# Kernel optimization log

Measured on AMD Instinct MI355X. Metric: run time of the kernel, lower is better.

The kernel has to match this reference:

```python
import jax, jax.numpy as jnp
import numpy as np

N_NODES = 100000
N_EDGES = 1600000
IN_FEAT = 50
HIDDEN = 64
N_CLASSES = 41


def setup_inputs() -> dict:
    key = jax.random.key(0)
    ks = jax.random.split(key, 8)
    x = jax.random.normal(ks[0], (N_NODES, IN_FEAT), dtype=jnp.float32)
    W1_l = jax.random.normal(ks[1], (IN_FEAT, HIDDEN), dtype=jnp.float32) * (1.0 / np.sqrt(IN_FEAT))
    W1_r = jax.random.normal(ks[2], (IN_FEAT, HIDDEN), dtype=jnp.float32) * (1.0 / np.sqrt(IN_FEAT))
    b1 = jnp.zeros((HIDDEN,), dtype=jnp.float32)
    W2_l = jax.random.normal(ks[3], (HIDDEN, N_CLASSES), dtype=jnp.float32) * (1.0 / np.sqrt(HIDDEN))
    W2_r = jax.random.normal(ks[4], (HIDDEN, N_CLASSES), dtype=jnp.float32) * (1.0 / np.sqrt(HIDDEN))
    b2 = jnp.zeros((N_CLASSES,), dtype=jnp.float32)
    src = jax.random.randint(ks[5], (N_EDGES,), 0, N_NODES, dtype=jnp.int64 if jax.config.jax_enable_x64 else jnp.int32)
    dst = jax.random.randint(ks[6], (N_EDGES,), 0, N_NODES, dtype=jnp.int64 if jax.config.jax_enable_x64 else jnp.int32)
    return {"x": x, "W1_l": W1_l, "W1_r": W1_r, "b1": b1,
            "W2_l": W2_l, "W2_r": W2_r, "b2": b2, "src": src, "dst": dst}


def _sage_conv(h, src, dst, W_l, W_r, b):
    # sum-aggregate neighbor features (message from src -> dst), then dense transform
    agg = jax.ops.segment_sum(h[src], dst, num_segments=N_NODES)  # [N, F]
    return agg @ W_l + h @ W_r + b


def reference(x, W1_l, W1_r, b1, W2_l, W2_r, b2, src, dst):
    h = _sage_conv(x, src, dst, W1_l, W1_r, b1)
    h = jax.nn.relu(h)
    # dropout is identity in eval mode
    o = _sage_conv(h, src, dst, W2_l, W2_r, b2)
    return jax.nn.log_softmax(o, axis=1)
```

## Files before the change

### kernel.cpp

```cpp
#include <hip/hip_runtime.h>
#include <hip/hip_bf16.h>
#include <math.h>

#define N_NODES   100000
#define N_EDGES   1600000
#define IN_FEAT   50
#define HIDDEN    64
#define N_CLASSES 41
#define NC48      48
#define N_TILES   (N_NODES / 16)

#define NPB   200
#define NBUK  (N_NODES / NPB)
#define BEPT  16
#define BA_BLOCKS ((N_EDGES + 256 * BEPT - 1) / (256 * BEPT))
#define SCAP  4096

typedef __attribute__((ext_vector_type(8))) _Float16 half8;
typedef __attribute__((ext_vector_type(4))) float   float4v;

union f16pk { _Float16 h[2]; unsigned u; };
union quadpk { uint4 v; _Float16 h[8]; };

__device__ __forceinline__ int clampidx(int i) {
  return ((unsigned)i < (unsigned)N_NODES) ? i : 0;
}

__device__ __forceinline__ void acc8(float* acc, const quadpk& u, float one) {
#pragma unroll
  for (int t = 0; t < 8; ++t) acc[t] = fmaf((float)u.h[t], one, acc[t]);
}

__global__ __launch_bounds__(256) void packx_kernel(
    const float* __restrict__ x, _Float16* __restrict__ xh) {
  int i = blockIdx.x * 256 + threadIdx.x;
  if (i >= N_NODES * 64) return;
  int node = i >> 6, c = i & 63;
  xh[i] = (c < IN_FEAT) ? (_Float16)x[node * IN_FEAT + c] : (_Float16)0.f;
}

__global__ __launch_bounds__(256) void packwts_kernel(
    const float* __restrict__ W1l, const float* __restrict__ W1r,
    const float* __restrict__ W2l, const float* __restrict__ W2r,
    unsigned* __restrict__ wt1l, unsigned* __restrict__ wt1r,
    unsigned* __restrict__ wt2l, unsigned* __restrict__ wt2r,
    int* __restrict__ bcnt) {
  if (blockIdx.x == 0) {
    for (int j = threadIdx.x; j < 512; j += 256) bcnt[j] = 0;
  }
  int i = blockIdx.x * 256 + threadIdx.x;
  f16pk pk;
  if (i < 2048 * 2) {
    int which = i >> 11, j = i & 2047;
    int n = j >> 5, kp = j & 31;
    const float* W = which ? W1r : W1l;
    int k0 = 2 * kp, k1 = 2 * kp + 1;
    pk.h[0] = (_Float16)((k0 < IN_FEAT) ? W[k0 * HIDDEN + n] : 0.f);
    pk.h[1] = (_Float16)((k1 < IN_FEAT) ? W[k1 * HIDDEN + n] : 0.f);
    (which ? wt1r : wt1l)[j] = pk.u;
  } else if (i < 4096 + 2 * 1536) {
    int j = i - 4096;
    int which = (j >= 1536), jj = which ? j - 1536 : j;
    int n = jj >> 5, kp = jj & 31;
    const float* W = which ? W2r : W2l;
    pk.h[0] = (_Float16)((n < N_CLASSES) ? W[(2 * kp) * N_CLASSES + n] : 0.f);
    pk.h[1] = (_Float16)((n < N_CLASSES) ? W[(2 * kp + 1) * N_CLASSES + n] : 0.f);
    (which ? wt2r : wt2l)[jj] = pk.u;
  }
}

__global__ __launch_bounds__(256) void bhist_kernel(
    const int* __restrict__ dst, int* __restrict__ bcnt) {
  __shared__ int lh[NBUK];
  int tid = threadIdx.x;
  for (int i = tid; i < NBUK; i += 256) lh[i] = 0;
  __syncthreads();
  int base = blockIdx.x * (256 * BEPT);
#pragma unroll
  for (int k = 0; k < BEPT; ++k) {
    int e = base + k * 256 + tid;
    if (e < N_EDGES) {
      int d = clampidx(dst[e]);
      atomicAdd(&lh[(unsigned)d / (unsigned)NPB], 1);
    }
  }
  __syncthreads();
  for (int i = tid; i < NBUK; i += 256)
    if (lh[i]) atomicAdd(&bcnt[i], lh[i]);
}

__global__ __launch_bounds__(256) void bscan_kernel(
    const int* __restrict__ bcnt, int* __restrict__ wbase,
    int* __restrict__ wcur, int* __restrict__ start) {
  __shared__ int lds[256];
  int tid = threadIdx.x;
  int i0 = 2 * tid, i1 = 2 * tid + 1;
  int a0 = (i0 < NBUK) ? bcnt[i0] : 0;
  int a1 = (i1 < NBUK) ? bcnt[i1] : 0;
  int s = a0 + a1;
  lds[tid] = s;
  __syncthreads();
  for (int off = 1; off < 256; off <<= 1) {
    int t = (tid >= off) ? lds[tid - off] : 0;
    __syncthreads();
    lds[tid] += t;
    __syncthreads();
  }
  int excl = lds[tid] - s;
  if (i0 < NBUK) { wbase[i0] = excl;      wcur[i0] = excl; }
  if (i1 < NBUK) { wbase[i1] = excl + a0; wcur[i1] = excl + a0; }
  if (tid == 0) { wbase[NBUK] = N_EDGES; start[N_NODES] = N_EDGES; }
}

__global__ __launch_bounds__(256) void bucketA_kernel(
    const int* __restrict__ src, const int* __restrict__ dst,
    int* __restrict__ wcur, int2* __restrict__ pairs) {
  __shared__ int lcnt[NBUK];
  __shared__ int lbase[NBUK];
  int tid = threadIdx.x;
  for (int i = tid; i < NBUK; i += 256) lcnt[i] = 0;
  __syncthreads();
  int base = blockIdx.x * (256 * BEPT);
  int s[BEPT], d[BEPT], rk[BEPT];
#pragma unroll
  for (int k = 0; k < BEPT; ++k) {
    int e = base + k * 256 + tid;
    rk[k] = -1;
    if (e < N_EDGES) {
      s[k] = src[e];
      d[k] = clampidx(dst[e]);
      int w = (unsigned)d[k] / (unsigned)NPB;
      rk[k] = atomicAdd(&lcnt[w], 1);
    }
  }
  __syncthreads();
  for (int i = tid; i < NBUK; i += 256)
    lbase[i] = atomicAdd(&wcur[i], lcnt[i]);
  __syncthreads();
#pragma unroll
  for (int k = 0; k < BEPT; ++k) {
    if (rk[k] >= 0) {
      int w = (unsigned)d[k] / (unsigned)NPB;
      int pos = lbase[w] + rk[k];
      if ((unsigned)pos < (unsigned)N_EDGES) {
        int2 p; p.x = s[k]; p.y = d[k];
        pairs[pos] = p;
      }
    }
  }
}

__global__ __launch_bounds__(256) void sort2_kernel(
    const int2* __restrict__ pairs, const int* __restrict__ wbase,
    int* __restrict__ start, int* __restrict__ ssrc) {
  __shared__ int obuf[SCAP];
  __shared__ int lhist[NPB];
  __shared__ int lcur[NPB];
  __shared__ int lscan[256];
  int b = blockIdx.x;
  int nbase = b * NPB;
  int lo = wbase[b];
  int hi = wbase[b + 1];
  int ne = hi - lo;
  int tid = threadIdx.x;
  for (int i = tid; i < NPB; i += 256) lhist[i] = 0;
  __syncthreads();
  for (int i = lo + tid; i < hi; i += 256) {
    int2 p = pairs[i];
    unsigned li = (unsigned)(p.y - nbase);
    if (li < (unsigned)NPB) atomicAdd(&lhist[li], 1);
  }
  __syncthreads();
  int hv = (tid < NPB) ? lhist[tid] : 0;
  lscan[tid] = hv;
  __syncthreads();
  for (int off = 1; off < 256; off <<= 1) {
    int t = (tid >= off) ? lscan[tid - off] : 0;
    __syncthreads();
    lscan[tid] += t;
    __syncthreads();
  }
  if (tid < NPB) {
    int excl = lscan[tid] - hv;
    lcur[tid] = excl;
    unsigned sidx = (unsigned)(nbase + tid);
    if (sidx < (unsigned)N_NODES) start[sidx] = lo + excl;
  }
  __syncthreads();
  if (ne >= 0 && ne <= SCAP) {
    for (int i = lo + tid; i < hi; i += 256) {
      int2 p = pairs[i];
      unsigned li = (unsigned)(p.y - nbase);
      if (li < (unsigned)NPB) {
        int pos = atomicAdd(&lcur[li], 1);
        if ((unsigned)pos < (unsigned)SCAP) obuf[pos] = p.x;
      }
    }
    __syncthreads();
    for (int i = tid; i < ne; i += 256) {
      unsigned gi = (unsigned)(lo + i);
      if (gi < (unsigned)N_EDGES) ssrc[gi] = obuf[i];
    }
  } else {
    for (int i = lo + tid; i < hi; i += 256) {
      int2 p = pairs[i];
      unsigned li = (unsigned)(p.y - nbase);
      if (li < (unsigned)NPB) {
        int pos = atomicAdd(&lcur[li], 1);
        unsigned gi = (unsigned)(lo + pos);
        if (gi < (unsigned)N_EDGES) ssrc[gi] = p.x;
      }
    }
  }
}

__global__ __launch_bounds__(256) void g1mlp_kernel(
    const uint4* __restrict__ xq,
    const int* __restrict__ start, const int* __restrict__ ssrc,
    const _Float16* __restrict__ xh,
    const unsigned* __restrict__ wt1l, const unsigned* __restrict__ wt1r,
    const unsigned* __restrict__ wt2l, const unsigned* __restrict__ wt2r,
    const float* __restrict__ b1, const float* __restrict__ b2,
    _Float16* __restrict__ hlh, float* __restrict__ opart, float one) {
  __shared__ float aggF[16][64];
  __shared__ float sH[16][68];
  int tile = blockIdx.x;
  int wv = threadIdx.x >> 6;
  int lane = threadIdx.x & 63;
  int r = lane >> 3, q = lane & 7;

  for (int k = 0; k < 4; ++k) {
    int node = tile * 16 + wv * 4 + k;

    float accA[8] = {0.f, 0.f, 0.f, 0.f, 0.f, 0.f, 0.f, 0.f};
    float accB[8] = {0.f, 0.f, 0.f, 0.f, 0.f, 0.f, 0.f, 0.f};

    int s0 = start[node], s1 = start[node + 1];
    for (int base = s0; base < s1; base += 64) {
      int cnt = s1 - base;
      if (cnt > 64) cnt = 64;
      int idxv = (lane < cnt) ? ssrc[base + lane] : 0;
      int j = 0;
      for (; j + 16 <= cnt; j += 16) {
        int iA = clampidx(__shfl(idxv, j + r));
        int iB = clampidx(__shfl(idxv, j + 8 + r));
        quadpk uA, uB;
        uA.v = xq[iA * 8 + q];
        uB.v = xq[iB * 8 + q];
        acc8(accA, uA, one);
        acc8(accB, uB, one);
      }
      for (; j + 8 <= cnt; j += 8) {
        int iA = clampidx(__shfl(idxv, j + r));
        quadpk uA;
        uA.v = xq[iA * 8 + q];
        acc8(accA, uA, one);
      }
      if (j < cnt) {
        int nrem = cnt - j;
        int iA = clampidx(__shfl(idxv, j + r));
        if (r < nrem) {
          quadpk uA;
          uA.v = xq[iA * 8 + q];
          acc8(accA, uA, one);
        }
      }
    }
#pragma unroll
    for (int t = 0; t < 8; ++t) accA[t] += accB[t];
#pragma unroll
    for (int off = 8; off <= 32; off <<= 1) {
#pragma unroll
      for (int t = 0; t < 8; ++t) accA[t] += __shfl_xor(accA[t], off);
    }
    if (r == 0) {
      int nl = wv * 4 + k;
#pragma unroll
      for (int t = 0; t < 8; ++t) aggF[nl][q * 8 + t] = accA[t];
    }
  }
  __syncthreads();

  if (wv != 0) return;
  int m = lane & 15, quad = lane >> 4;

  half8 Aa[2], Ax[2];
#pragma unroll
  for (int s = 0; s < 2; ++s) {
    const float* pa = &aggF[m][s * 32 + quad * 8];
    half8 A;
#pragma unroll
    for (int jj = 0; jj < 8; ++jj) A[jj] = (_Float16)pa[jj];
    Aa[s] = A;
    Ax[s] = *(const half8*)(xh + (tile * 16 + m) * 64 + s * 32 + quad * 8);
  }

#pragma unroll
  for (int t = 0; t < 4; ++t) {
    int n = t * 16 + m;
    half8 Bl0 = *(const half8*)(wt1l + n * 32 + quad * 4);
    half8 Bl1 = *(const half8*)(wt1l + n * 32 + 16 + quad * 4);
    half8 Br0 = *(const half8*)(wt1r + n * 32 + quad * 4);
    half8 Br1 = *(const half8*)(wt1r + n * 32 + 16 + quad * 4);
    float4v acc = {0.f, 0.f, 0.f, 0.f};
    acc = __builtin_amdgcn_mfma_f32_16x16x32_f16(Aa[0], Bl0, acc, 0, 0, 0);
    acc = __builtin_amdgcn_mfma_f32_16x16x32_f16(Aa[1], Bl1, acc, 0, 0, 0);
    acc = __builtin_amdgcn_mfma_f32_16x16x32_f16(Ax[0], Br0, acc, 0, 0, 0);
    acc = __builtin_amdgcn_mfma_f32_16x16x32_f16(Ax[1], Br1, acc, 0, 0, 0);
    float bv = b1[n];
#pragma unroll
    for (int rr = 0; rr < 4; ++rr) {
      sH[quad * 4 + rr][n] = fmaxf(acc[rr] + bv, 0.f);
    }
  }

  half8 Ah[2];
#pragma unroll
  for (int s = 0; s < 2; ++s) {
    const float* pr = &sH[m][s * 32 + quad * 8];
    half8 A;
#pragma unroll
    for (int jj = 0; jj < 8; ++jj) A[jj] = (_Float16)pr[jj];
    Ah[s] = A;
  }

#pragma unroll
  for (int t = 0; t < 3; ++t) {
    int n = t * 16 + m;
    half8 Cl0 = *(const half8*)(wt2l + n * 32 + quad * 4);
    half8 Cl1 = *(const half8*)(wt2l + n * 32 + 16 + quad * 4);
    half8 Cr0 = *(const half8*)(wt2r + n * 32 + quad * 4);
    half8 Cr1 = *(const half8*)(wt2r + n * 32 + 16 + quad * 4);
    float4v acc2 = {0.f, 0.f, 0.f, 0.f};
    float4v acc3 = {0.f, 0.f, 0.f, 0.f};
    acc2 = __builtin_amdgcn_mfma_f32_16x16x32_f16(Ah[0], Cl0, acc2, 0, 0, 0);
    acc2 = __builtin_amdgcn_mfma_f32_16x16x32_f16(Ah[1], Cl1, acc2, 0, 0, 0);
    acc3 = __builtin_amdgcn_mfma_f32_16x16x32_f16(Ah[0], Cr0, acc3, 0, 0, 0);
    acc3 = __builtin_amdgcn_mfma_f32_16x16x32_f16(Ah[1], Cr1, acc3, 0, 0, 0);
    float bv = (n < N_CLASSES) ? b2[n] : 0.f;
#pragma unroll
    for (int rr = 0; rr < 4; ++rr) {
      int row = tile * 16 + quad * 4 + rr;
      hlh[row * NC48 + n] = (_Float16)acc2[rr];
      opart[row * NC48 + n] = acc3[rr] + bv;
    }
  }
}

__global__ __launch_bounds__(256) void gather2_kernel(
    const uint4* __restrict__ hq,
    const float4* __restrict__ opart4,
    const int* __restrict__ start, const int* __restrict__ ssrc,
    float* __restrict__ out, float one) {
  int node = (blockIdx.x * 256 + threadIdx.x) >> 6;
  if (node >= N_NODES) return;
  int lane = threadIdx.x & 63;
  int r = lane >> 3, q = lane & 7;
  bool qOK = (q < 6);

  float op[8] = {0.f, 0.f, 0.f, 0.f, 0.f, 0.f, 0.f, 0.f};
  if (r == 0 && qOK) {
    float4 a = opart4[node * 12 + q * 2];
    float4 b = opart4[node * 12 + q * 2 + 1];
    op[0] = a.x; op[1] = a.y; op[2] = a.z; op[3] = a.w;
    op[4] = b.x; op[5] = b.y; op[6] = b.z; op[7] = b.w;
  }

  float accA[8] = {0.f, 0.f, 0.f, 0.f, 0.f, 0.f, 0.f, 0.f};
  float accB[8] = {0.f, 0.f, 0.f, 0.f, 0.f, 0.f, 0.f, 0.f};

  int s0 = start[node], s1 = start[node + 1];
  for (int base = s0; base < s1; base += 64) {
    int cnt = s1 - base;
    if (cnt > 64) cnt = 64;
    int idxv = (lane < cnt) ? ssrc[base + lane] : 0;
    int j = 0;
    for (; j + 16 <= cnt; j += 16) {
      int iA = clampidx(__shfl(idxv, j + r));
      int iB = clampidx(__shfl(idxv, j + 8 + r));
      if (qOK) {
        quadpk uA, uB;
        uA.v = hq[iA * 6 + q];
        uB.v = hq[iB * 6 + q];
        acc8(accA, uA, one);
        acc8(accB, uB, one);
      }
    }
    for (; j + 8 <= cnt; j += 8) {
      int iA = clampidx(__shfl(idxv, j + r));
      if (qOK) {
        quadpk uA;
        uA.v = hq[iA * 6 + q];
        acc8(accA, uA, one);
      }
    }
    if (j < cnt) {
      int nrem = cnt - j;
      int iA = clampidx(__shfl(idxv, j + r));
      if (r < nrem && qOK) {
        quadpk uA;
        uA.v = hq[iA * 6 + q];
        acc8(accA, uA, one);
      }
    }
  }
#pragma unroll
  for (int t = 0; t < 8; ++t) accA[t] += accB[t];
#pragma unroll
  for (int off = 8; off <= 32; off <<= 1) {
#pragma unroll
    for (int t = 0; t < 8; ++t) accA[t] += __shfl_xor(accA[t], off);
  }

  bool own = (r == 0) && qOK;
  float o[8];
  float lmax = -INFINITY;
#pragma unroll
  for (int t = 0; t < 8; ++t) {
    int f = q * 8 + t;
    o[t] = op[t] + accA[t];
    if (own && f < N_CLASSES) lmax = fmaxf(lmax, o[t]);
  }
  float vm = own ? lmax : -INFINITY;
#pragma unroll
  for (int off = 4; off >= 1; off >>= 1) vm = fmaxf(vm, __shfl_xor(vm, off));
  float lsum = 0.f;
#pragma unroll
  for (int t = 0; t < 8; ++t) {
    int f = q * 8 + t;
    if (own && f < N_CLASSES) lsum += expf(o[t] - vm);
  }
#pragma unroll
  for (int off = 4; off >= 1; off >>= 1) lsum += __shfl_xor(lsum, off);
  float lse = logf(lsum);
  if (own) {
#pragma unroll
    for (int t = 0; t < 8; ++t) {
      int f = q * 8 + t;
      if (f < N_CLASSES) out[node * N_CLASSES + f] = o[t] - vm - lse;
    }
  }
}

extern "C" void kernel_launch(void* const* d_in, const int* in_sizes, int n_in,
                              void* d_out, int out_size, void* d_ws, size_t ws_size,
                              hipStream_t stream) {
  const float* x   = (const float*)d_in[0];
  const float* W1l = (const float*)d_in[1];
  const float* W1r = (const float*)d_in[2];
  const float* b1  = (const float*)d_in[3];
  const float* W2l = (const float*)d_in[4];
  const float* W2r = (const float*)d_in[5];
  const float* b2  = (const float*)d_in[6];
  const int*   src = (const int*)d_in[7];
  const int*   dst = (const int*)d_in[8];
  float* out = (float*)d_out;

  int* counts  = (int*)d_ws;
  int* start   = counts + N_NODES;
  int* cursor  = start + (N_NODES + 1);
  int* partial = cursor + N_NODES;
  int* ssrc    = partial + 64;
  unsigned* wt1l = (unsigned*)(ssrc + N_EDGES);
  unsigned* wt1r = wt1l + 2048;
  unsigned* wt2l = wt1r + 2048;
  unsigned* wt2r = wt2l + 1536;
  uintptr_t pal = ((uintptr_t)(wt2r + 1536) + 255) & ~(uintptr_t)255;
  float* opart   = (float*)pal;
  _Float16* xh   = (_Float16*)(opart + (size_t)N_NODES * NC48);
  _Float16* hlh  = xh + (size_t)N_NODES * 64;

  int* bcnt  = counts;
  int* wbase = counts + 512;

  int2* pairs = (int2*)opart;
  int*  wcur  = (int*)(pairs + N_EDGES);

  packx_kernel<<<(N_NODES * 64 + 255) / 256, 256, 0, stream>>>(x, xh);
  packwts_kernel<<<(7168 + 255) / 256, 256, 0, stream>>>(
      W1l, W1r, W2l, W2r, wt1l, wt1r, wt2l, wt2r, bcnt);
  bhist_kernel<<<BA_BLOCKS, 256, 0, stream>>>(dst, bcnt);
  bscan_kernel<<<1, 256, 0, stream>>>(bcnt, wbase, wcur, start);
  bucketA_kernel<<<BA_BLOCKS, 256, 0, stream>>>(src, dst, wcur, pairs);
  sort2_kernel<<<NBUK, 256, 0, stream>>>(pairs, wbase, start, ssrc);

  g1mlp_kernel<<<N_TILES, 256, 0, stream>>>(
      (const uint4*)xh, start, ssrc, xh, wt1l, wt1r, wt2l, wt2r,
      b1, b2, hlh, opart, 1.0f);

  int gblocks = (N_NODES * 64 + 255) / 256;
  gather2_kernel<<<gblocks, 256, 0, stream>>>(
      (const uint4*)hlh, (const float4*)opart, start, ssrc, out, 1.0f);
}
```

Baseline: 248.6 us.

## Pack edge pairs into single ints and simplify gather index loading

Bucketing now stores each edge as one 32-bit word, with the source node in the upper bits and the destination's offset within its bucket in the low 8 bits. This halves the intermediate pair traffic written by bucketA and read twice by sort2. Both gather kernels drop the 64-wide index load plus shuffle broadcast and instead have each lane group load its edge index directly, 16 edges per step. This removes the shuffles and the remainder loops, at the cost of redundant per-lane index loads.

```diff
diff --git a/kernel.cpp b/kernel.cpp
--- a/kernel.cpp
+++ b/kernel.cpp
@@ -114,23 +114,24 @@
 
 __global__ __launch_bounds__(256) void bucketA_kernel(
     const int* __restrict__ src, const int* __restrict__ dst,
-    int* __restrict__ wcur, int2* __restrict__ pairs) {
+    int* __restrict__ wcur, int* __restrict__ pairs) {
   __shared__ int lcnt[NBUK];
   __shared__ int lbase[NBUK];
   int tid = threadIdx.x;
   for (int i = tid; i < NBUK; i += 256) lcnt[i] = 0;
   __syncthreads();
   int base = blockIdx.x * (256 * BEPT);
-  int s[BEPT], d[BEPT], rk[BEPT];
+  int pk[BEPT], w[BEPT], rk[BEPT];
 #pragma unroll
   for (int k = 0; k < BEPT; ++k) {
     int e = base + k * 256 + tid;
     rk[k] = -1;
     if (e < N_EDGES) {
-      s[k] = src[e];
-      d[k] = clampidx(dst[e]);
-      int w = (unsigned)d[k] / (unsigned)NPB;
-      rk[k] = atomicAdd(&lcnt[w], 1);
+      int s = clampidx(src[e]);
+      int d = clampidx(dst[e]);
+      w[k] = (unsigned)d / (unsigned)NPB;
+      pk[k] = (s << 8) | (d - w[k] * NPB);
+      rk[k] = atomicAdd(&lcnt[w[k]], 1);
     }
   }
   __syncthreads();
@@ -140,18 +141,14 @@
 #pragma unroll
   for (int k = 0; k < BEPT; ++k) {
     if (rk[k] >= 0) {
-      int w = (unsigned)d[k] / (unsigned)NPB;
-      int pos = lbase[w] + rk[k];
-      if ((unsigned)pos < (unsigned)N_EDGES) {
-        int2 p; p.x = s[k]; p.y = d[k];
-        pairs[pos] = p;
-      }
+      int pos = lbase[w[k]] + rk[k];
+      if ((unsigned)pos < (unsigned)N_EDGES) pairs[pos] = pk[k];
     }
   }
 }
 
 __global__ __launch_bounds__(256) void sort2_kernel(
-    const int2* __restrict__ pairs, const int* __restrict__ wbase,
+    const int* __restrict__ pairs, const int* __restrict__ wbase,
     int* __restrict__ start, int* __restrict__ ssrc) {
   __shared__ int obuf[SCAP];
   __shared__ int lhist[NPB];
@@ -166,8 +163,7 @@
   for (int i = tid; i < NPB; i += 256) lhist[i] = 0;
   __syncthreads();
   for (int i = lo + tid; i < hi; i += 256) {
-    int2 p = pairs[i];
-    unsigned li = (unsigned)(p.y - nbase);
+    unsigned li = (unsigned)pairs[i] & 255u;
     if (li < (unsigned)NPB) atomicAdd(&lhist[li], 1);
   }
   __syncthreads();
@@ -189,11 +185,11 @@
   __syncthreads();
   if (ne >= 0 && ne <= SCAP) {
     for (int i = lo + tid; i < hi; i += 256) {
-      int2 p = pairs[i];
-      unsigned li = (unsigned)(p.y - nbase);
+      int p = pairs[i];
+      unsigned li = (unsigned)p & 255u;
       if (li < (unsigned)NPB) {
         int pos = atomicAdd(&lcur[li], 1);
-        if ((unsigned)pos < (unsigned)SCAP) obuf[pos] = p.x;
+        if ((unsigned)pos < (unsigned)SCAP) obuf[pos] = (int)((unsigned)p >> 8);
       }
     }
     __syncthreads();
@@ -203,12 +199,12 @@
     }
   } else {
     for (int i = lo + tid; i < hi; i += 256) {
-      int2 p = pairs[i];
-      unsigned li = (unsigned)(p.y - nbase);
+      int p = pairs[i];
+      unsigned li = (unsigned)p & 255u;
       if (li < (unsigned)NPB) {
         int pos = atomicAdd(&lcur[li], 1);
         unsigned gi = (unsigned)(lo + pos);
-        if (gi < (unsigned)N_EDGES) ssrc[gi] = p.x;
+        if (gi < (unsigned)N_EDGES) ssrc[gi] = (int)((unsigned)p >> 8);
       }
     }
   }
@@ -236,34 +232,17 @@
     float accB[8] = {0.f, 0.f, 0.f, 0.f, 0.f, 0.f, 0.f, 0.f};
 
     int s0 = start[node], s1 = start[node + 1];
-    for (int base = s0; base < s1; base += 64) {
-      int cnt = s1 - base;
-      if (cnt > 64) cnt = 64;
-      int idxv = (lane < cnt) ? ssrc[base + lane] : 0;
-      int j = 0;
-      for (; j + 16 <= cnt; j += 16) {
-        int iA = clampidx(__shfl(idxv, j + r));
-        int iB = clampidx(__shfl(idxv, j + 8 + r));
-        quadpk uA, uB;
-        uA.v = xq[iA * 8 + q];
-        uB.v = xq[iB * 8 + q];
-        acc8(accA, uA, one);
-        acc8(accB, uB, one);
-      }
-      for (; j + 8 <= cnt; j += 8) {
-        int iA = clampidx(__shfl(idxv, j + r));
-        quadpk uA;
-        uA.v = xq[iA * 8 + q];
+    for (int base = s0; base < s1; base += 16) {
+      int eA = base + r, eB = base + 8 + r;
+      if (eA < s1) {
+        int iA = clampidx(ssrc[eA]);
+        quadpk uA; uA.v = xq[iA * 8 + q];
         acc8(accA, uA, one);
       }
-      if (j < cnt) {
-        int nrem = cnt - j;
-        int iA = clampidx(__shfl(idxv, j + r));
-        if (r < nrem) {
-          quadpk uA;
-          uA.v = xq[iA * 8 + q];
-          acc8(accA, uA, one);
-        }
+      if (eB < s1) {
+        int iB = clampidx(ssrc[eB]);
+        quadpk uB; uB.v = xq[iB * 8 + q];
+        acc8(accB, uB, one);
       }
     }
 #pragma unroll
@@ -370,38 +349,17 @@
   float accB[8] = {0.f, 0.f, 0.f, 0.f, 0.f, 0.f, 0.f, 0.f};
 
   int s0 = start[node], s1 = start[node + 1];
-  for (int base = s0; base < s1; base += 64) {
-    int cnt = s1 - base;
-    if (cnt > 64) cnt = 64;
-    int idxv = (lane < cnt) ? ssrc[base + lane] : 0;
-    int j = 0;
-    for (; j + 16 <= cnt; j += 16) {
-      int iA = clampidx(__shfl(idxv, j + r));
-      int iB = clampidx(__shfl(idxv, j + 8 + r));
-      if (qOK) {
-        quadpk uA, uB;
-        uA.v = hq[iA * 6 + q];
-        uB.v = hq[iB * 6 + q];
-        acc8(accA, uA, one);
-        acc8(accB, uB, one);
-      }
-    }
-    for (; j + 8 <= cnt; j += 8) {
-      int iA = clampidx(__shfl(idxv, j + r));
-      if (qOK) {
-        quadpk uA;
-        uA.v = hq[iA * 6 + q];
-        acc8(accA, uA, one);
-      }
-    }
-    if (j < cnt) {
-      int nrem = cnt - j;
-      int iA = clampidx(__shfl(idxv, j + r));
-      if (r < nrem && qOK) {
-        quadpk uA;
-        uA.v = hq[iA * 6 + q];
-        acc8(accA, uA, one);
-      }
+  for (int base = s0; base < s1; base += 16) {
+    int eA = base + r, eB = base + 8 + r;
+    if (eA < s1 && qOK) {
+      int iA = clampidx(ssrc[eA]);
+      quadpk uA; uA.v = hq[iA * 6 + q];
+      acc8(accA, uA, one);
+    }
+    if (eB < s1 && qOK) {
+      int iB = clampidx(ssrc[eB]);
+      quadpk uB; uB.v = hq[iB * 6 + q];
+      acc8(accB, uB, one);
     }
   }
 #pragma unroll
@@ -473,8 +431,8 @@
   int* bcnt  = counts;
   int* wbase = counts + 512;
 
-  int2* pairs = (int2*)opart;
-  int*  wcur  = (int*)(pairs + N_EDGES);
+  int* pairs = (int*)opart;
+  int* wcur  = pairs + N_EDGES;
 
   packx_kernel<<<(N_NODES * 64 + 255) / 256, 256, 0, stream>>>(x, xh);
   packwts_kernel<<<(7168 + 255) / 256, 256, 0, stream>>>(
```

Result: slower. 286.2 us (+15.1%).

## Fuse prep kernels, drop bucket scan launch, pack edge pairs into one int

Applied to the files above, without the earlier changes.

Merges the x-pack and weight-pack kernels into a single prep launch and removes the standalone single-block bucket scan by recomputing the bucket prefix sum redundantly inside bucketA and sort2 blocks. Edge pairs are packed into one 32-bit word (src shifted left by 8, local dst offset in the low bits), which halves the traffic for writing and reading the intermediate pairs buffer. It also pads the aggF shared array to 68 columns to avoid bank conflicts. In exchange, every block repeats a 256-wide scan, and the packing relies on src fitting in 24 bits.

```diff
diff --git a/kernel.cpp b/kernel.cpp
--- a/kernel.cpp
+++ b/kernel.cpp
@@ -16,6 +16,9 @@
 #define BA_BLOCKS ((N_EDGES + 256 * BEPT - 1) / (256 * BEPT))
 #define SCAP  4096
 
+#define PACKX_BLOCKS (N_NODES * 64 / 256)
+#define PW_BLOCKS    28
+
 typedef __attribute__((ext_vector_type(8))) _Float16 half8;
 typedef __attribute__((ext_vector_type(4))) float   float4v;
 
@@ -31,24 +34,27 @@
   for (int t = 0; t < 8; ++t) acc[t] = fmaf((float)u.h[t], one, acc[t]);
 }
 
-__global__ __launch_bounds__(256) void packx_kernel(
-    const float* __restrict__ x, _Float16* __restrict__ xh) {
-  int i = blockIdx.x * 256 + threadIdx.x;
-  if (i >= N_NODES * 64) return;
-  int node = i >> 6, c = i & 63;
-  xh[i] = (c < IN_FEAT) ? (_Float16)x[node * IN_FEAT + c] : (_Float16)0.f;
-}
-
-__global__ __launch_bounds__(256) void packwts_kernel(
+__global__ __launch_bounds__(256) void prep_kernel(
+    const float* __restrict__ x, _Float16* __restrict__ xh,
     const float* __restrict__ W1l, const float* __restrict__ W1r,
     const float* __restrict__ W2l, const float* __restrict__ W2r,
     unsigned* __restrict__ wt1l, unsigned* __restrict__ wt1r,
     unsigned* __restrict__ wt2l, unsigned* __restrict__ wt2r,
-    int* __restrict__ bcnt) {
-  if (blockIdx.x == 0) {
-    for (int j = threadIdx.x; j < 512; j += 256) bcnt[j] = 0;
-  }
-  int i = blockIdx.x * 256 + threadIdx.x;
+    int* __restrict__ bcnt, int* __restrict__ wcurrel,
+    int* __restrict__ start) {
+  if (blockIdx.x < PACKX_BLOCKS) {
+    int i = blockIdx.x * 256 + threadIdx.x;
+    int node = i >> 6, c = i & 63;
+    xh[i] = (c < IN_FEAT) ? (_Float16)x[node * IN_FEAT + c] : (_Float16)0.f;
+    return;
+  }
+  int tid = threadIdx.x;
+  if (blockIdx.x == PACKX_BLOCKS) {
+    bcnt[tid] = 0; bcnt[256 + tid] = 0;
+    wcurrel[tid] = 0; wcurrel[256 + tid] = 0;
+    if (tid == 0) start[N_NODES] = N_EDGES;
+  }
+  int i = (blockIdx.x - PACKX_BLOCKS) * 256 + tid;
   f16pk pk;
   if (i < 2048 * 2) {
     int which = i >> 11, j = i & 2047;
@@ -89,85 +95,95 @@
     if (lh[i]) atomicAdd(&bcnt[i], lh[i]);
 }
 
-__global__ __launch_bounds__(256) void bscan_kernel(
-    const int* __restrict__ bcnt, int* __restrict__ wbase,
-    int* __restrict__ wcur, int* __restrict__ start) {
-  __shared__ int lds[256];
+__global__ __launch_bounds__(256) void bucketA_kernel(
+    const int* __restrict__ src, const int* __restrict__ dst,
+    const int* __restrict__ bcnt, int* __restrict__ wcurrel,
+    int* __restrict__ pairs) {
+  __shared__ int sc[256];
+  __shared__ int wb[NBUK];
+  __shared__ int lcnt[NBUK];
+  __shared__ int lbase[NBUK];
   int tid = threadIdx.x;
   int i0 = 2 * tid, i1 = 2 * tid + 1;
   int a0 = (i0 < NBUK) ? bcnt[i0] : 0;
   int a1 = (i1 < NBUK) ? bcnt[i1] : 0;
   int s = a0 + a1;
-  lds[tid] = s;
+  sc[tid] = s;
+  for (int i = tid; i < NBUK; i += 256) lcnt[i] = 0;
   __syncthreads();
   for (int off = 1; off < 256; off <<= 1) {
-    int t = (tid >= off) ? lds[tid - off] : 0;
+    int t = (tid >= off) ? sc[tid - off] : 0;
     __syncthreads();
-    lds[tid] += t;
+    sc[tid] += t;
     __syncthreads();
   }
-  int excl = lds[tid] - s;
-  if (i0 < NBUK) { wbase[i0] = excl;      wcur[i0] = excl; }
-  if (i1 < NBUK) { wbase[i1] = excl + a0; wcur[i1] = excl + a0; }
-  if (tid == 0) { wbase[NBUK] = N_EDGES; start[N_NODES] = N_EDGES; }
-}
-
-__global__ __launch_bounds__(256) void bucketA_kernel(
-    const int* __restrict__ src, const int* __restrict__ dst,
-    int* __restrict__ wcur, int2* __restrict__ pairs) {
-  __shared__ int lcnt[NBUK];
-  __shared__ int lbase[NBUK];
-  int tid = threadIdx.x;
-  for (int i = tid; i < NBUK; i += 256) lcnt[i] = 0;
-  __syncthreads();
+  int excl = sc[tid] - s;
+  if (i0 < NBUK) wb[i0] = excl;
+  if (i1 < NBUK) wb[i1] = excl + a0;
+  __syncthreads();
+
   int base = blockIdx.x * (256 * BEPT);
-  int s[BEPT], d[BEPT], rk[BEPT];
+  int pk[BEPT], w[BEPT], rk[BEPT];
 #pragma unroll
   for (int k = 0; k < BEPT; ++k) {
     int e = base + k * 256 + tid;
     rk[k] = -1;
     if (e < N_EDGES) {
-      s[k] = src[e];
-      d[k] = clampidx(dst[e]);
-      int w = (unsigned)d[k] / (unsigned)NPB;
-      rk[k] = atomicAdd(&lcnt[w], 1);
+      int sv = clampidx(src[e]);
+      int d = clampidx(dst[e]);
+      w[k] = (unsigned)d / (unsigned)NPB;
+      pk[k] = (sv << 8) | (d - w[k] * NPB);
+      rk[k] = atomicAdd(&lcnt[w[k]], 1);
     }
   }
   __syncthreads();
   for (int i = tid; i < NBUK; i += 256)
-    lbase[i] = atomicAdd(&wcur[i], lcnt[i]);
+    lbase[i] = wb[i] + atomicAdd(&wcurrel[i], lcnt[i]);
   __syncthreads();
 #pragma unroll
   for (int k = 0; k < BEPT; ++k) {
     if (rk[k] >= 0) {
-      int w = (unsigned)d[k] / (unsigned)NPB;
-      int pos = lbase[w] + rk[k];
-      if ((unsigned)pos < (unsigned)N_EDGES) {
-        int2 p; p.x = s[k]; p.y = d[k];
-        pairs[pos] = p;
-      }
+      int pos = lbase[w[k]] + rk[k];
+      if ((unsigned)pos < (unsigned)N_EDGES) pairs[pos] = pk[k];
     }
   }
 }
 
 __global__ __launch_bounds__(256) void sort2_kernel(
-    const int2* __restrict__ pairs, const int* __restrict__ wbase,
+    const int* __restrict__ pairs, const int* __restrict__ bcnt,
     int* __restrict__ start, int* __restrict__ ssrc) {
   __shared__ int obuf[SCAP];
   __shared__ int lhist[NPB];
   __shared__ int lcur[NPB];
   __shared__ int lscan[256];
+  __shared__ int lohi[2];
   int b = blockIdx.x;
   int nbase = b * NPB;
-  int lo = wbase[b];
-  int hi = wbase[b + 1];
-  int ne = hi - lo;
   int tid = threadIdx.x;
+  {
+    int i0 = 2 * tid, i1 = 2 * tid + 1;
+    int a0 = (i0 < NBUK) ? bcnt[i0] : 0;
+    int a1 = (i1 < NBUK) ? bcnt[i1] : 0;
+    int s = a0 + a1;
+    lscan[tid] = s;
+    __syncthreads();
+    for (int off = 1; off < 256; off <<= 1) {
+      int t = (tid >= off) ? lscan[tid - off] : 0;
+      __syncthreads();
+      lscan[tid] += t;
+      __syncthreads();
+    }
+    int excl = lscan[tid] - s;
+    if (i0 == b) { lohi[0] = excl;      lohi[1] = a0; }
+    if (i1 == b) { lohi[0] = excl + a0; lohi[1] = a1; }
+  }
   for (int i = tid; i < NPB; i += 256) lhist[i] = 0;
   __syncthreads();
+  int lo = lohi[0];
+  int ne = lohi[1];
+  int hi = lo + ne;
   for (int i = lo + tid; i < hi; i += 256) {
-    int2 p = pairs[i];
-    unsigned li = (unsigned)(p.y - nbase);
+    unsigned li = (unsigned)pairs[i] & 255u;
     if (li < (unsigned)NPB) atomicAdd(&lhist[li], 1);
   }
   __syncthreads();
@@ -189,11 +205,11 @@
   __syncthreads();
   if (ne >= 0 && ne <= SCAP) {
     for (int i = lo + tid; i < hi; i += 256) {
-      int2 p = pairs[i];
-      unsigned li = (unsigned)(p.y - nbase);
+      int p = pairs[i];
+      unsigned li = (unsigned)p & 255u;
       if (li < (unsigned)NPB) {
         int pos = atomicAdd(&lcur[li], 1);
-        if ((unsigned)pos < (unsigned)SCAP) obuf[pos] = p.x;
+        if ((unsigned)pos < (unsigned)SCAP) obuf[pos] = (int)((unsigned)p >> 8);
       }
     }
     __syncthreads();
@@ -203,12 +219,12 @@
     }
   } else {
     for (int i = lo + tid; i < hi; i += 256) {
-      int2 p = pairs[i];
-      unsigned li = (unsigned)(p.y - nbase);
+      int p = pairs[i];
+      unsigned li = (unsigned)p & 255u;
       if (li < (unsigned)NPB) {
         int pos = atomicAdd(&lcur[li], 1);
         unsigned gi = (unsigned)(lo + pos);
-        if (gi < (unsigned)N_EDGES) ssrc[gi] = p.x;
+        if (gi < (unsigned)N_EDGES) ssrc[gi] = (int)((unsigned)p >> 8);
       }
     }
   }
@@ -222,7 +238,7 @@
     const unsigned* __restrict__ wt2l, const unsigned* __restrict__ wt2r,
     const float* __restrict__ b1, const float* __restrict__ b2,
     _Float16* __restrict__ hlh, float* __restrict__ opart, float one) {
-  __shared__ float aggF[16][64];
+  __shared__ float aggF[16][68];
   __shared__ float sH[16][68];
   int tile = blockIdx.x;
   int wv = threadIdx.x >> 6;
@@ -470,19 +486,17 @@
   _Float16* xh   = (_Float16*)(opart + (size_t)N_NODES * NC48);
   _Float16* hlh  = xh + (size_t)N_NODES * 64;
 
-  int* bcnt  = counts;
-  int* wbase = counts + 512;
-
-  int2* pairs = (int2*)opart;
-  int*  wcur  = (int*)(pairs + N_EDGES);
-
-  packx_kernel<<<(N_NODES * 64 + 255) / 256, 256, 0, stream>>>(x, xh);
-  packwts_kernel<<<(7168 + 255) / 256, 256, 0, stream>>>(
-      W1l, W1r, W2l, W2r, wt1l, wt1r, wt2l, wt2r, bcnt);
+  int* bcnt    = counts;
+  int* wcurrel = counts + 512;
+
+  int* pairs = (int*)opart;
+
+  prep_kernel<<<PACKX_BLOCKS + PW_BLOCKS, 256, 0, stream>>>(
+      x, xh, W1l, W1r, W2l, W2r, wt1l, wt1r, wt2l, wt2r,
+      bcnt, wcurrel, start);
   bhist_kernel<<<BA_BLOCKS, 256, 0, stream>>>(dst, bcnt);
-  bscan_kernel<<<1, 256, 0, stream>>>(bcnt, wbase, wcur, start);
-  bucketA_kernel<<<BA_BLOCKS, 256, 0, stream>>>(src, dst, wcur, pairs);
-  sort2_kernel<<<NBUK, 256, 0, stream>>>(pairs, wbase, start, ssrc);
+  bucketA_kernel<<<BA_BLOCKS, 256, 0, stream>>>(src, dst, bcnt, wcurrel, pairs);
+  sort2_kernel<<<NBUK, 256, 0, stream>>>(pairs, bcnt, start, ssrc);
 
   g1mlp_kernel<<<N_TILES, 256, 0, stream>>>(
       (const uint4*)xh, start, ssrc, xh, wt1l, wt1r, wt2l, wt2r,
```

After: 250.4 us. Within noise of the previous version (+0.7%).
